# Kernel tuning notes

Measured on AMD Instinct MI355X. Metric: run time of the kernel, lower is better.

The kernel has to match this reference:

```python
import jax, jax.numpy as jnp
import numpy as np

B, N, F, C = 8, 1024, 2048, 4
H = F // 2

def setup_inputs() -> dict:
    key = jax.random.key(0)
    k0, k1, k2 = jax.random.split(key, 3)
    vectors = jax.random.normal(k0, (B, N, F), jnp.float32)  # pooled per-mask backbone features
    W1 = jax.random.normal(k1, (H, 2 * F), jnp.float32) * np.float32(1.0 / np.sqrt(2 * F))
    b1 = jnp.zeros((H,), jnp.float32)
    W2 = jax.random.normal(k2, (C, H), jnp.float32) * np.float32(1.0 / np.sqrt(H))
    b2 = jnp.zeros((C,), jnp.float32)
    return {"vectors": vectors, "W1": W1, "b1": b1, "W2": W2, "b2": b2}

def reference(vectors, W1, b1, W2, b2):
    # Original: for each pair (i, j): sigmoid(L2(L1(cat(v_i, v_j)))).
    # There is NO nonlinearity between the two Linears, so the composition is
    # exactly linear in (v_i, v_j):
    #   logits[b,i,j] = W2 @ (W1a v_i + W1b v_j + b1) + b2
    # which factors into two per-node projections + a pairwise broadcast add,
    # avoiding the [B,N,N,H] intermediate.
    f = vectors.shape[-1]
    W1a, W1b = W1[:, :f], W1[:, f:]
    p1 = jnp.einsum('bnh,ch->bnc', jnp.einsum('bnf,hf->bnh', vectors, W1a), W2)  # [B,N,C]
    p2 = jnp.einsum('bnh,ch->bnc', jnp.einsum('bnf,hf->bnh', vectors, W1b), W2)  # [B,N,C]
    const = W2 @ b1 + b2  # [C]
    logits = p1[:, :, None, :] + p2[:, None, :, :] + const  # [B, i, j, C]
    # torch code stacks j along dim=2 and i along dim=3 -> connections[b,c,j,i]
    connections = jax.nn.sigmoid(logits).transpose(0, 3, 2, 1)  # [B, C, N_j, N_i]
    return vectors, connections
```

## Files before the change

kernel.cpp:

```cpp
#include <hip/hip_runtime.h>
#include <hip/hip_bf16.h>

#define BB 8
#define NN 1024
#define FF 2048
#define CC 4
#define HH 1024
#define ROWS (BB * NN)
#define HCHUNKS 16
#define MELEMS (8 * FF)

__device__ __forceinline__ float sigmoidf_fast(float x) {
    return __builtin_amdgcn_rcpf(1.0f + __expf(-x));
}

__global__ __launch_bounds__(256) void k_fold_partial(const float* __restrict__ W1,
                                                      const float* __restrict__ W2,
                                                      float* __restrict__ Mpart) {
    int k = blockIdx.x * 256 + threadIdx.x;
    int chunk = blockIdx.y;
    int half = k >> 11;
    int f = k & (FF - 1);
    const float* col = W1 + (size_t)k;
    int h0 = chunk * (HH / HCHUNKS);
    float a0 = 0.f, a1 = 0.f, a2 = 0.f, a3 = 0.f;
    #pragma unroll 4
    for (int h = h0; h < h0 + (HH / HCHUNKS); ++h) {
        float wv = col[(size_t)h * (2 * FF)];
        a0 += wv * W2[0 * HH + h];
        a1 += wv * W2[1 * HH + h];
        a2 += wv * W2[2 * HH + h];
        a3 += wv * W2[3 * HH + h];
    }
    float* mp = Mpart + (size_t)chunk * MELEMS + (size_t)(half * 4) * FF + f;
    mp[0 * FF] = a0;
    mp[1 * FF] = a1;
    mp[2 * FF] = a2;
    mp[3 * FF] = a3;
}

__global__ __launch_bounds__(256) void k_fold_reduce(const float* __restrict__ Mpart,
                                                     const float* __restrict__ W2,
                                                     const float* __restrict__ b1,
                                                     const float* __restrict__ b2,
                                                     float* __restrict__ M,
                                                     float* __restrict__ cst) {
    if (blockIdx.x < 64) {
        int idx = blockIdx.x * 256 + threadIdx.x;
        float s = 0.f;
        #pragma unroll
        for (int p = 0; p < HCHUNKS; ++p) s += Mpart[(size_t)p * MELEMS + idx];
        M[idx] = s;
    } else {
        int t = threadIdx.x;
        int c = t >> 6, lane = t & 63;
        float s = 0.f;
        for (int h = lane; h < HH; h += 64) s += W2[c * HH + h] * b1[h];
        #pragma unroll
        for (int off = 32; off; off >>= 1) s += __shfl_down(s, off);
        if (lane == 0) cst[c] = s + b2[c];
    }
}

#define ROWS_PER_BLOCK 8
__global__ __launch_bounds__(256) void k_pcompute(const float* __restrict__ v,
                                                  const float* __restrict__ M,
                                                  float* __restrict__ outv,
                                                  float* __restrict__ P1,
                                                  float* __restrict__ P2) {
    int t = threadIdx.x;
    int f0 = t * 8;
    float w[8][8];
    #pragma unroll
    for (int j = 0; j < 8; ++j) {
        float4 a = *(const float4*)(M + j * FF + f0);
        float4 b = *(const float4*)(M + j * FF + f0 + 4);
        w[j][0] = a.x; w[j][1] = a.y; w[j][2] = a.z; w[j][3] = a.w;
        w[j][4] = b.x; w[j][5] = b.y; w[j][6] = b.z; w[j][7] = b.w;
    }
    __shared__ float red[4 * 8];
    int row0 = blockIdx.x * ROWS_PER_BLOCK;
    for (int r = 0; r < ROWS_PER_BLOCK; ++r) {
        int row = row0 + r;
        const float* vr = v + (size_t)row * FF + f0;
        float4 a = *(const float4*)vr;
        float4 b = *(const float4*)(vr + 4);
        *(float4*)(outv + (size_t)row * FF + f0) = a;
        *(float4*)(outv + (size_t)row * FF + f0 + 4) = b;
        float x[8] = {a.x, a.y, a.z, a.w, b.x, b.y, b.z, b.w};
        float acc[8];
        #pragma unroll
        for (int j = 0; j < 8; ++j) {
            float s = 0.f;
            #pragma unroll
            for (int k = 0; k < 8; ++k) s += x[k] * w[j][k];
            acc[j] = s;
        }
        #pragma unroll
        for (int j = 0; j < 8; ++j) {
            float s = acc[j];
            #pragma unroll
            for (int off = 32; off; off >>= 1) s += __shfl_down(s, off);
            acc[j] = s;
        }
        int lane = t & 63, wv = t >> 6;
        if (lane == 0) {
            #pragma unroll
            for (int j = 0; j < 8; ++j) red[wv * 8 + j] = acc[j];
        }
        __syncthreads();
        if (t < 8) {
            float s = red[t] + red[8 + t] + red[16 + t] + red[24 + t];
            if (t < 4) P1[t * ROWS + row] = s;
            else       P2[(t - 4) * ROWS + row] = s;
        }
        __syncthreads();
    }
}

__global__ __launch_bounds__(256) void k_conn(const float* __restrict__ P1,
                                              const float* __restrict__ P2,
                                              const float* __restrict__ cst,
                                              float* __restrict__ out) {
    const int nrows = BB * CC * NN;
    for (int r = blockIdx.x; r < nrows; r += gridDim.x) {
        int b = r >> 12;
        int c = (r >> 10) & 3;
        int j = r & (NN - 1);
        float s = P2[c * ROWS + b * NN + j] + cst[c];
        const float4* p1 = (const float4*)(P1 + c * ROWS + b * NN);
        float4* o = (float4*)(out + (size_t)r * NN);
        int t = threadIdx.x;
        float4 p = p1[t];
        float4 rs;
        rs.x = sigmoidf_fast(p.x + s);
        rs.y = sigmoidf_fast(p.y + s);
        rs.z = sigmoidf_fast(p.z + s);
        rs.w = sigmoidf_fast(p.w + s);
        o[t] = rs;
    }
}

extern "C" void kernel_launch(void* const* d_in, const int* in_sizes, int n_in,
                              void* d_out, int out_size, void* d_ws, size_t ws_size,
                              hipStream_t stream) {
    const float* vectors = (const float*)d_in[0];
    const float* W1 = (const float*)d_in[1];
    const float* b1 = (const float*)d_in[2];
    const float* W2 = (const float*)d_in[3];
    const float* b2 = (const float*)d_in[4];

    float* out_vectors = (float*)d_out;
    float* out_conn = (float*)d_out + (size_t)ROWS * FF;

    float* w = (float*)d_ws;
    float* Mpart = w;
    float* M     = Mpart + HCHUNKS * MELEMS;
    float* cst   = M + MELEMS;
    float* P1    = cst + 16;
    float* P2    = P1 + CC * ROWS;

    k_fold_partial<<<dim3(16, HCHUNKS), 256, 0, stream>>>(W1, W2, Mpart);
    k_fold_reduce<<<65, 256, 0, stream>>>(Mpart, W2, b1, b2, M, cst);
    k_pcompute<<<ROWS / ROWS_PER_BLOCK, 256, 0, stream>>>(vectors, M, out_vectors, P1, P2);
    k_conn<<<2048, 256, 0, stream>>>(P1, P2, cst, out_conn);
}
```

Measured before the change: 77.73 us.

## Vectorize weight fold, butterfly reductions, nontemporal streaming, fold bias into P2

The weight-folding kernel now loads float4 columns with nontemporal loads and picks 32 or 64 H-chunks when the workspace is large enough. The per-row projection uses an 8-way butterfly shuffle that reduces all eight outputs in one pass and handles four rows per barrier pair. The bias constant is added into P2 once, so the pairwise kernel does one fewer add and load per row. Output writes use nontemporal stores and the pairwise grid grows to 8192 blocks. The main targets are launch and reduction overhead and cache pollution from the large streaming writes. More chunks mean more partial-sum traffic in the reduce step.

```diff
diff --git a/kernel.cpp b/kernel.cpp
--- a/kernel.cpp
+++ b/kernel.cpp
@@ -7,49 +7,79 @@
 #define CC 4
 #define HH 1024
 #define ROWS (BB * NN)
-#define HCHUNKS 16
 #define MELEMS (8 * FF)
+
+typedef float f4 __attribute__((ext_vector_type(4)));
 
 __device__ __forceinline__ float sigmoidf_fast(float x) {
     return __builtin_amdgcn_rcpf(1.0f + __expf(-x));
 }
 
-__global__ __launch_bounds__(256) void k_fold_partial(const float* __restrict__ W1,
-                                                      const float* __restrict__ W2,
-                                                      float* __restrict__ Mpart) {
-    int k = blockIdx.x * 256 + threadIdx.x;
+__device__ __forceinline__ float butterfly8(float a[8], int lane) {
+    #pragma unroll
+    for (int i = 0; i < 4; ++i) {
+        float send = (lane & 1) ? a[i] : a[i + 4];
+        float got = __shfl_xor(send, 1, 64);
+        a[i] = ((lane & 1) ? a[i + 4] : a[i]) + got;
+    }
+    #pragma unroll
+    for (int i = 0; i < 2; ++i) {
+        float send = (lane & 2) ? a[i] : a[i + 2];
+        float got = __shfl_xor(send, 2, 64);
+        a[i] = ((lane & 2) ? a[i + 2] : a[i]) + got;
+    }
+    {
+        float send = (lane & 4) ? a[0] : a[1];
+        float got = __shfl_xor(send, 4, 64);
+        a[0] = ((lane & 4) ? a[1] : a[0]) + got;
+    }
+    a[0] += __shfl_xor(a[0], 8, 64);
+    a[0] += __shfl_xor(a[0], 16, 64);
+    a[0] += __shfl_xor(a[0], 32, 64);
+    return a[0];
+}
+
+__global__ __launch_bounds__(256) void k_fold(const float* __restrict__ W1,
+                                              const float* __restrict__ W2,
+                                              float* __restrict__ Mpart,
+                                              int hper) {
+    int k4 = (blockIdx.x * 256 + threadIdx.x) << 2;
     int chunk = blockIdx.y;
-    int half = k >> 11;
-    int f = k & (FF - 1);
-    const float* col = W1 + (size_t)k;
-    int h0 = chunk * (HH / HCHUNKS);
-    float a0 = 0.f, a1 = 0.f, a2 = 0.f, a3 = 0.f;
+    int half = k4 >> 11;
+    int f = k4 & (FF - 1);
+    int h0 = chunk * hper;
+    f4 a0 = {0.f, 0.f, 0.f, 0.f}, a1 = a0, a2 = a0, a3 = a0;
+    const float* base = W1 + (size_t)h0 * (2 * FF) + k4;
     #pragma unroll 4
-    for (int h = h0; h < h0 + (HH / HCHUNKS); ++h) {
-        float wv = col[(size_t)h * (2 * FF)];
-        a0 += wv * W2[0 * HH + h];
-        a1 += wv * W2[1 * HH + h];
-        a2 += wv * W2[2 * HH + h];
-        a3 += wv * W2[3 * HH + h];
+    for (int i = 0; i < hper; ++i) {
+        f4 wv = __builtin_nontemporal_load((const f4*)(base + (size_t)i * (2 * FF)));
+        int h = h0 + i;
+        float s0 = W2[0 * HH + h], s1 = W2[1 * HH + h];
+        float s2 = W2[2 * HH + h], s3 = W2[3 * HH + h];
+        a0 += wv * s0;
+        a1 += wv * s1;
+        a2 += wv * s2;
+        a3 += wv * s3;
     }
     float* mp = Mpart + (size_t)chunk * MELEMS + (size_t)(half * 4) * FF + f;
-    mp[0 * FF] = a0;
-    mp[1 * FF] = a1;
-    mp[2 * FF] = a2;
-    mp[3 * FF] = a3;
-}
-
-__global__ __launch_bounds__(256) void k_fold_reduce(const float* __restrict__ Mpart,
-                                                     const float* __restrict__ W2,
-                                                     const float* __restrict__ b1,
-                                                     const float* __restrict__ b2,
-                                                     float* __restrict__ M,
-                                                     float* __restrict__ cst) {
+    *(f4*)(mp + 0 * FF) = a0;
+    *(f4*)(mp + 1 * FF) = a1;
+    *(f4*)(mp + 2 * FF) = a2;
+    *(f4*)(mp + 3 * FF) = a3;
+}
+
+__global__ __launch_bounds__(256) void k_reduce(const float* __restrict__ Mpart,
+                                                const float* __restrict__ W2,
+                                                const float* __restrict__ b1,
+                                                const float* __restrict__ b2,
+                                                float* __restrict__ M,
+                                                float* __restrict__ cst,
+                                                int nchunks) {
     if (blockIdx.x < 64) {
         int idx = blockIdx.x * 256 + threadIdx.x;
         float s = 0.f;
-        #pragma unroll
-        for (int p = 0; p < HCHUNKS; ++p) s += Mpart[(size_t)p * MELEMS + idx];
+        #pragma unroll 8
+        for (int p = 0; p < nchunks; ++p) s += Mpart[(size_t)p * MELEMS + idx];
         M[idx] = s;
     } else {
         int t = threadIdx.x;
@@ -62,82 +92,84 @@
     }
 }
 
-#define ROWS_PER_BLOCK 8
 __global__ __launch_bounds__(256) void k_pcompute(const float* __restrict__ v,
                                                   const float* __restrict__ M,
+                                                  const float* __restrict__ cst,
                                                   float* __restrict__ outv,
                                                   float* __restrict__ P1,
-                                                  float* __restrict__ P2) {
+                                                  float* __restrict__ P2f) {
     int t = threadIdx.x;
+    int lane = t & 63, wvi = t >> 6;
     int f0 = t * 8;
     float w[8][8];
     #pragma unroll
     for (int j = 0; j < 8; ++j) {
-        float4 a = *(const float4*)(M + j * FF + f0);
-        float4 b = *(const float4*)(M + j * FF + f0 + 4);
-        w[j][0] = a.x; w[j][1] = a.y; w[j][2] = a.z; w[j][3] = a.w;
-        w[j][4] = b.x; w[j][5] = b.y; w[j][6] = b.z; w[j][7] = b.w;
-    }
-    __shared__ float red[4 * 8];
-    int row0 = blockIdx.x * ROWS_PER_BLOCK;
-    for (int r = 0; r < ROWS_PER_BLOCK; ++r) {
-        int row = row0 + r;
-        const float* vr = v + (size_t)row * FF + f0;
-        float4 a = *(const float4*)vr;
-        float4 b = *(const float4*)(vr + 4);
-        *(float4*)(outv + (size_t)row * FF + f0) = a;
-        *(float4*)(outv + (size_t)row * FF + f0 + 4) = b;
-        float x[8] = {a.x, a.y, a.z, a.w, b.x, b.y, b.z, b.w};
-        float acc[8];
+        f4 a = *(const f4*)(M + j * FF + f0);
+        f4 b = *(const f4*)(M + j * FF + f0 + 4);
+        w[j][0] = a[0]; w[j][1] = a[1]; w[j][2] = a[2]; w[j][3] = a[3];
+        w[j][4] = b[0]; w[j][5] = b[1]; w[j][6] = b[2]; w[j][7] = b[3];
+    }
+    int vidx = ((lane & 1) << 2) | (lane & 2) | ((lane >> 2) & 1);
+    __shared__ float red[4][32];
+    int row0 = blockIdx.x * 8;
+
+    #pragma unroll
+    for (int batch = 0; batch < 2; ++batch) {
+        float fin[4];
         #pragma unroll
-        for (int j = 0; j < 8; ++j) {
-            float s = 0.f;
+        for (int r = 0; r < 4; ++r) {
+            int row = row0 + batch * 4 + r;
+            const f4* vr = (const f4*)(v + (size_t)row * FF + f0);
+            f4 a = __builtin_nontemporal_load(vr);
+            f4 b = __builtin_nontemporal_load(vr + 1);
+            f4* po = (f4*)(outv + (size_t)row * FF + f0);
+            __builtin_nontemporal_store(a, po);
+            __builtin_nontemporal_store(b, po + 1);
+            float x[8] = {a[0], a[1], a[2], a[3], b[0], b[1], b[2], b[3]};
+            float acc[8];
             #pragma unroll
-            for (int k = 0; k < 8; ++k) s += x[k] * w[j][k];
-            acc[j] = s;
+            for (int j = 0; j < 8; ++j) {
+                float s = 0.f;
+                #pragma unroll
+                for (int k = 0; k < 8; ++k) s += x[k] * w[j][k];
+                acc[j] = s;
+            }
+            fin[r] = butterfly8(acc, lane);
         }
-        #pragma unroll
-        for (int j = 0; j < 8; ++j) {
-            float s = acc[j];
+        if (lane < 8) {
             #pragma unroll
-            for (int off = 32; off; off >>= 1) s += __shfl_down(s, off);
-            acc[j] = s;
-        }
-        int lane = t & 63, wv = t >> 6;
-        if (lane == 0) {
-            #pragma unroll
-            for (int j = 0; j < 8; ++j) red[wv * 8 + j] = acc[j];
+            for (int r = 0; r < 4; ++r) red[r][wvi * 8 + vidx] = fin[r];
         }
         __syncthreads();
-        if (t < 8) {
-            float s = red[t] + red[8 + t] + red[16 + t] + red[24 + t];
-            if (t < 4) P1[t * ROWS + row] = s;
-            else       P2[(t - 4) * ROWS + row] = s;
+        if (t < 32) {
+            int r = t >> 3, j = t & 7;
+            float s = red[r][j] + red[r][8 + j] + red[r][16 + j] + red[r][24 + j];
+            int row = row0 + batch * 4 + r;
+            if (j < 4) P1[j * ROWS + row] = s;
+            else       P2f[(j - 4) * ROWS + row] = s + cst[j - 4];
         }
         __syncthreads();
     }
 }
 
 __global__ __launch_bounds__(256) void k_conn(const float* __restrict__ P1,
-                                              const float* __restrict__ P2,
-                                              const float* __restrict__ cst,
+                                              const float* __restrict__ P2f,
                                               float* __restrict__ out) {
+    int t = threadIdx.x;
     const int nrows = BB * CC * NN;
     for (int r = blockIdx.x; r < nrows; r += gridDim.x) {
         int b = r >> 12;
         int c = (r >> 10) & 3;
         int j = r & (NN - 1);
-        float s = P2[c * ROWS + b * NN + j] + cst[c];
-        const float4* p1 = (const float4*)(P1 + c * ROWS + b * NN);
-        float4* o = (float4*)(out + (size_t)r * NN);
-        int t = threadIdx.x;
-        float4 p = p1[t];
-        float4 rs;
-        rs.x = sigmoidf_fast(p.x + s);
-        rs.y = sigmoidf_fast(p.y + s);
-        rs.z = sigmoidf_fast(p.z + s);
-        rs.w = sigmoidf_fast(p.w + s);
-        o[t] = rs;
+        float s = P2f[c * ROWS + b * NN + j];
+        const f4* p1 = (const f4*)(P1 + c * ROWS + b * NN);
+        f4 p = p1[t];
+        f4 rs;
+        rs[0] = sigmoidf_fast(p[0] + s);
+        rs[1] = sigmoidf_fast(p[1] + s);
+        rs[2] = sigmoidf_fast(p[2] + s);
+        rs[3] = sigmoidf_fast(p[3] + s);
+        __builtin_nontemporal_store(rs, (f4*)(out + (size_t)r * NN) + t);
     }
 }
 
@@ -153,15 +185,23 @@
     float* out_vectors = (float*)d_out;
     float* out_conn = (float*)d_out + (size_t)ROWS * FF;
 
+    int nchunks = 16;
+    {
+        size_t fixed = (size_t)MELEMS + 16 + 2 * (size_t)CC * ROWS;
+        if (ws_size >= ((size_t)64 * MELEMS + fixed) * sizeof(float)) nchunks = 64;
+        else if (ws_size >= ((size_t)32 * MELEMS + fixed) * sizeof(float)) nchunks = 32;
+    }
+    int hper = HH / nchunks;
+
     float* w = (float*)d_ws;
     float* Mpart = w;
-    float* M     = Mpart + HCHUNKS * MELEMS;
+    float* M     = Mpart + (size_t)nchunks * MELEMS;
     float* cst   = M + MELEMS;
     float* P1    = cst + 16;
-    float* P2    = P1 + CC * ROWS;
-
-    k_fold_partial<<<dim3(16, HCHUNKS), 256, 0, stream>>>(W1, W2, Mpart);
-    k_fold_reduce<<<65, 256, 0, stream>>>(Mpart, W2, b1, b2, M, cst);
-    k_pcompute<<<ROWS / ROWS_PER_BLOCK, 256, 0, stream>>>(vectors, M, out_vectors, P1, P2);
-    k_conn<<<2048, 256, 0, stream>>>(P1, P2, cst, out_conn);
-}
+    float* P2f   = P1 + (size_t)CC * ROWS;
+
+    k_fold<<<dim3(4, nchunks), 256, 0, stream>>>(W1, W2, Mpart, hper);
+    k_reduce<<<65, 256, 0, stream>>>(Mpart, W2, b1, b2, M, cst, nchunks);
+    k_pcompute<<<ROWS / 8, 256, 0, stream>>>(vectors, M, cst, out_vectors, P1, P2f);
+    k_conn<<<8192, 256, 0, stream>>>(P1, P2f, out_conn);
+}
```

After: 79.17 us. No clear change (+1.9%).
